# Kernel optimization log

Measured on AMD Instinct MI355X. Metric: run time of the kernel, lower is better.

## Reference

```python
import jax, jax.numpy as jnp
import numpy as np
import math

B, H, N, T, D, R = 1, 32, 2048, 2048, 128, 64


def setup_inputs() -> dict:
    key = jax.random.key(0)
    k1, k2, k3, k4 = jax.random.split(key, 4)
    q = jax.random.normal(k1, (B, H, N, D), dtype=jnp.float32)
    k_orig = jax.random.normal(k2, (B, H, T, D), dtype=jnp.float32)
    # emulate a quantized key: orig + small perturbation (any float tensor works)
    k_quant = k_orig + 0.05 * jax.random.normal(k3, (B, H, T, D), dtype=jnp.float32)
    # JL projection buffer: randn(dim, rank) / sqrt(rank)
    G = jax.random.normal(k4, (D, R), dtype=jnp.float32) / math.sqrt(R)
    return {"q": q, "k_orig": k_orig, "k_quant": k_quant, "G": G}


def reference(q, k_orig, k_quant, G):
    rank = G.shape[1]
    alpha = 1.0 / math.sqrt(rank)
    # compute_sign: sign of JL-projected residual -> (B,H,T,R), values in {-1,0,+1}
    e = k_orig - k_quant
    s = jnp.sign(jnp.einsum('bhtd,dr->bhtr', e, G))
    # correct_score
    raw_scores = jnp.einsum('bhnd,bhtd->bhnt', q, k_quant)          # (B,H,N,T)
    q_proj = jnp.einsum('bhnd,dr->bhnr', q, G) / math.sqrt(rank)     # (B,H,N,R)
    corr = jnp.einsum('bhnr,bhtr->bhnt', q_proj, s) * alpha          # (B,H,N,T)
    return raw_scores + corr
```

## Files before the change

kernel.cpp:

```cpp
#include <hip/hip_runtime.h>


#define H 32
#define NQ 2048
#define NT 2048
#define D 128
#define R 64
#define KDIM 192

typedef __attribute__((ext_vector_type(4))) float f32x4;
typedef __attribute__((ext_vector_type(8))) short bf16x8;

__device__ __forceinline__ short f2bf(float x) {
  union { float f; unsigned u; } v; v.f = x;
  unsigned r = v.u + 0x7fff + ((v.u >> 16) & 1);
  return (short)(r >> 16);
}
__device__ __forceinline__ float bf2f(short h) {
  union { unsigned u; float f; } v; v.u = ((unsigned)(unsigned short)h) << 16;
  return v.f;
}

__device__ __forceinline__ void gl_lds16(const void* g, void* l) {
  __builtin_amdgcn_global_load_lds(
      (const __attribute__((address_space(1))) void*)g,
      (__attribute__((address_space(3))) void*)l, 16, 0, 0);
}

__global__ __launch_bounds__(256, 2) void prep(
    const float* __restrict__ q, const float* __restrict__ ko,
    const float* __restrict__ kq, const float* __restrict__ G,
    short* __restrict__ Qb, short* __restrict__ Kb) {
  const int tid = threadIdx.x, lane = tid & 63, wave = tid >> 6;
  const int quad = lane >> 4, mrow = lane & 15;
  const bool kmode = blockIdx.x < (H * NT / 128);
  const long blk = kmode ? blockIdx.x : (blockIdx.x - H * NT / 128);
  const long rbase = blk * 128 + wave * 32;
  short* outb = kmode ? Kb : Qb;

  f32x4 acc[2][4] = {};

  for (int ks = 0; ks < 4; ++ks) {
    const int d0 = ks * 32 + quad * 8;
    bf16x8 gh[4], gl[4];
#pragma unroll
    for (int j = 0; j < 4; ++j) {
      const float* gp = G + (size_t)d0 * R + j * 16 + mrow;
#pragma unroll
      for (int e = 0; e < 8; ++e) {
        float g = gp[(size_t)e * R];
        short hb = f2bf(g);
        gh[j][e] = hb;
        gl[j][e] = f2bf(g - bf2f(hb));
      }
    }
    bf16x8 ah[2], al[2];
#pragma unroll
    for (int i = 0; i < 2; ++i) {
      const long row = rbase + i * 16 + mrow;
      if (kmode) {
        const f32x4 a0 = *(const f32x4*)(ko + row * D + d0);
        const f32x4 a1 = *(const f32x4*)(ko + row * D + d0 + 4);
        const f32x4 b0 = *(const f32x4*)(kq + row * D + d0);
        const f32x4 b1 = *(const f32x4*)(kq + row * D + d0 + 4);
        bf16x8 kqb;
#pragma unroll
        for (int t = 0; t < 4; ++t) {
          kqb[t] = f2bf(b0[t]); kqb[t + 4] = f2bf(b1[t]);
          float e0 = a0[t] - b0[t];
          short h0 = f2bf(e0); ah[i][t] = h0; al[i][t] = f2bf(e0 - bf2f(h0));
          float e1 = a1[t] - b1[t];
          short h1 = f2bf(e1); ah[i][t + 4] = h1; al[i][t + 4] = f2bf(e1 - bf2f(h1));
        }
        *(bf16x8*)(Kb + row * KDIM + d0) = kqb;
      } else {
        const f32x4 a0 = *(const f32x4*)(q + row * D + d0);
        const f32x4 a1 = *(const f32x4*)(q + row * D + d0 + 4);
        bf16x8 qb;
#pragma unroll
        for (int t = 0; t < 4; ++t) {
          short h0 = f2bf(a0[t]); qb[t] = h0; ah[i][t] = h0; al[i][t] = 0;
          short h1 = f2bf(a1[t]); qb[t + 4] = h1; ah[i][t + 4] = h1; al[i][t + 4] = 0;
        }
        *(bf16x8*)(Qb + row * KDIM + d0) = qb;
      }
    }
#pragma unroll
    for (int i = 0; i < 2; ++i)
#pragma unroll
      for (int j = 0; j < 4; ++j) {
        acc[i][j] = __builtin_amdgcn_mfma_f32_16x16x32_bf16(ah[i], gh[j], acc[i][j], 0, 0, 0);
        if (kmode) {
          acc[i][j] = __builtin_amdgcn_mfma_f32_16x16x32_bf16(al[i], gh[j], acc[i][j], 0, 0, 0);
          acc[i][j] = __builtin_amdgcn_mfma_f32_16x16x32_bf16(ah[i], gl[j], acc[i][j], 0, 0, 0);
        }
      }
  }
#pragma unroll
  for (int i = 0; i < 2; ++i)
#pragma unroll
    for (int j = 0; j < 4; ++j)
#pragma unroll
      for (int r = 0; r < 4; ++r) {
        const long row = rbase + i * 16 + quad * 4 + r;
        const int col = j * 16 + mrow;
        float v = acc[i][j][r];
        short s;
        if (kmode)
          s = v > 0.f ? (short)0x3C80 : (v < 0.f ? (short)0xBC80 : (short)0);
        else
          s = f2bf(v);
        outb[row * KDIM + 128 + col] = s;
      }
}

__global__ __launch_bounds__(256, 3) void gemm_bt(const short* __restrict__ Qb,
                                                  const short* __restrict__ Kb,
                                                  float* __restrict__ out) {
  const int h  = blockIdx.z;
  const int m0 = blockIdx.y * 128;
  const int n0 = blockIdx.x * 128;
  const short* A = Qb + (size_t)h * NQ * KDIM;
  const short* B = Kb + (size_t)h * NT * KDIM;

  __shared__ __align__(16) short As[2][128 * 32];
  __shared__ __align__(16) short Bs[2][128 * 32];

  const int tid = threadIdx.x, lane = tid & 63, wave = tid >> 6;
  const int wm = (wave >> 1) * 64, wn = (wave & 1) * 64;
  const int quad = lane >> 4, mrow = lane & 15;

  f32x4 acc[4][4] = {};

  const int srow = tid >> 2;
  const int scol = (tid & 3) * 8;
  const short* gA  = A + (size_t)(m0 + srow) * KDIM + scol;
  const short* gA2 = A + (size_t)(m0 + 64 + srow) * KDIM + scol;
  const short* gB  = B + (size_t)(n0 + srow) * KDIM + scol;
  const short* gB2 = B + (size_t)(n0 + 64 + srow) * KDIM + scol;

  auto stage = [&](int b, int kt) {
    char* a1 = (char*)(&As[b][0]) + wave * 1024;
    char* a2 = (char*)(&As[b][0]) + 4096 + wave * 1024;
    char* b1 = (char*)(&Bs[b][0]) + wave * 1024;
    char* b2 = (char*)(&Bs[b][0]) + 4096 + wave * 1024;
    gl_lds16(gA + kt * 32, a1);
    gl_lds16(gA2 + kt * 32, a2);
    gl_lds16(gB + kt * 32, b1);
    gl_lds16(gB2 + kt * 32, b2);
  };

  stage(0, 0);
  asm volatile("s_waitcnt vmcnt(0)" ::: "memory");
  __builtin_amdgcn_s_barrier();

#pragma unroll
  for (int kt = 0; kt < 6; ++kt) {
    const int cur = kt & 1;
    if (kt < 5) stage(cur ^ 1, kt + 1);

    bf16x8 af[4], bfv[4];
#pragma unroll
    for (int i = 0; i < 4; ++i) {
      af[i]  = *(const bf16x8*)((const char*)(&As[cur][0]) + (wm + i * 16 + mrow) * 64 + quad * 16);
      bfv[i] = *(const bf16x8*)((const char*)(&Bs[cur][0]) + (wn + i * 16 + mrow) * 64 + quad * 16);
    }
#pragma unroll
    for (int i = 0; i < 4; ++i)
#pragma unroll
      for (int j = 0; j < 4; ++j)
        acc[i][j] = __builtin_amdgcn_mfma_f32_16x16x32_bf16(af[i], bfv[j], acc[i][j], 0, 0, 0);

    if (kt < 5) {
      asm volatile("s_waitcnt vmcnt(0)" ::: "memory");
      __builtin_amdgcn_s_barrier();
    }
  }

  float* orow = out + ((size_t)h * NQ + m0) * NT + n0;
#pragma unroll
  for (int i = 0; i < 4; ++i)
#pragma unroll
    for (int r = 0; r < 4; ++r) {
      const int row = wm + i * 16 + quad * 4 + r;
      float* p = orow + (size_t)row * NT + wn + mrow;
#pragma unroll
      for (int j = 0; j < 4; ++j) p[j * 16] = acc[i][j][r];
    }
}

extern "C" void kernel_launch(void* const* d_in, const int* in_sizes, int n_in,
                              void* d_out, int out_size, void* d_ws, size_t ws_size,
                              hipStream_t stream) {
  const float* q  = (const float*)d_in[0];
  const float* ko = (const float*)d_in[1];
  const float* kq = (const float*)d_in[2];
  const float* G  = (const float*)d_in[3];
  float* out = (float*)d_out;

  short* Kb = (short*)d_ws;
  short* Qb = Kb + (size_t)H * NT * KDIM;

  prep<<<(H * NT + H * NQ) / 128, 256, 0, stream>>>(q, ko, kq, G, Qb, Kb);

  dim3 grid(NT / 128, NQ / 128, H);
  gemm_bt<<<grid, 256, 0, stream>>>(Qb, Kb, out);
}
```

Before: 678.6 us.

## Replace LDS-tiled GEMM with register-resident A strip streaming over all K tiles

The GEMM now launches 512 blocks of 512 threads. Each block owns a 128-row Q strip for one head and holds the full 192-wide A fragments in registers. It loops over all 16 key tiles, loading B fragments directly from global memory with a two-half software prefetch, and writes each 128x128 output tile with nontemporal stores. This removes LDS staging, barriers and repeated A loads, and the block index is swizzled so heads interleave. The cost is heavy register pressure and uncoalesced direct global B loads that depend on cache reuse across waves.

After: 684.9 us. No clear change (+0.9%).

```diff
diff --git a/kernel.cpp b/kernel.cpp
--- a/kernel.cpp
+++ b/kernel.cpp
@@ -19,12 +19,6 @@
 __device__ __forceinline__ float bf2f(short h) {
   union { unsigned u; float f; } v; v.u = ((unsigned)(unsigned short)h) << 16;
   return v.f;
-}
-
-__device__ __forceinline__ void gl_lds16(const void* g, void* l) {
-  __builtin_amdgcn_global_load_lds(
-      (const __attribute__((address_space(1))) void*)g,
-      (__attribute__((address_space(3))) void*)l, 16, 0, 0);
 }
 
 __global__ __launch_bounds__(256, 2) void prep(
@@ -114,79 +108,86 @@
       }
 }
 
-__global__ __launch_bounds__(256, 3) void gemm_bt(const short* __restrict__ Qb,
-                                                  const short* __restrict__ Kb,
-                                                  float* __restrict__ out) {
-  const int h  = blockIdx.z;
-  const int m0 = blockIdx.y * 128;
-  const int n0 = blockIdx.x * 128;
+__global__ __launch_bounds__(512, 2) void gemm_strip(const short* __restrict__ Qb,
+                                                     const short* __restrict__ Kb,
+                                                     float* __restrict__ out) {
+  const int bid = blockIdx.x;
+  const int h = (bid & 7) + ((bid >> 3) & 3) * 8;
+  const int m0 = (bid >> 5) * 128;
+
+  const int tid = threadIdx.x, lane = tid & 63, wave = tid >> 6;
+  const int quad = lane >> 4, mrow = lane & 15;
+  const int wm = (wave >> 2) * 64;
+  const int wn = (wave & 3) * 32;
+
   const short* A = Qb + (size_t)h * NQ * KDIM;
   const short* B = Kb + (size_t)h * NT * KDIM;
 
-  __shared__ __align__(16) short As[2][128 * 32];
-  __shared__ __align__(16) short Bs[2][128 * 32];
-
-  const int tid = threadIdx.x, lane = tid & 63, wave = tid >> 6;
-  const int wm = (wave >> 1) * 64, wn = (wave & 1) * 64;
-  const int quad = lane >> 4, mrow = lane & 15;
-
-  f32x4 acc[4][4] = {};
-
-  const int srow = tid >> 2;
-  const int scol = (tid & 3) * 8;
-  const short* gA  = A + (size_t)(m0 + srow) * KDIM + scol;
-  const short* gA2 = A + (size_t)(m0 + 64 + srow) * KDIM + scol;
-  const short* gB  = B + (size_t)(n0 + srow) * KDIM + scol;
-  const short* gB2 = B + (size_t)(n0 + 64 + srow) * KDIM + scol;
-
-  auto stage = [&](int b, int kt) {
-    char* a1 = (char*)(&As[b][0]) + wave * 1024;
-    char* a2 = (char*)(&As[b][0]) + 4096 + wave * 1024;
-    char* b1 = (char*)(&Bs[b][0]) + wave * 1024;
-    char* b2 = (char*)(&Bs[b][0]) + 4096 + wave * 1024;
-    gl_lds16(gA + kt * 32, a1);
-    gl_lds16(gA2 + kt * 32, a2);
-    gl_lds16(gB + kt * 32, b1);
-    gl_lds16(gB2 + kt * 32, b2);
-  };
-
-  stage(0, 0);
-  asm volatile("s_waitcnt vmcnt(0)" ::: "memory");
-  __builtin_amdgcn_s_barrier();
-
-#pragma unroll
-  for (int kt = 0; kt < 6; ++kt) {
-    const int cur = kt & 1;
-    if (kt < 5) stage(cur ^ 1, kt + 1);
-
-    bf16x8 af[4], bfv[4];
-#pragma unroll
-    for (int i = 0; i < 4; ++i) {
-      af[i]  = *(const bf16x8*)((const char*)(&As[cur][0]) + (wm + i * 16 + mrow) * 64 + quad * 16);
-      bfv[i] = *(const bf16x8*)((const char*)(&Bs[cur][0]) + (wn + i * 16 + mrow) * 64 + quad * 16);
+  bf16x8 af[4][6];
+#pragma unroll
+  for (int i = 0; i < 4; ++i) {
+    const short* ap = A + (size_t)(m0 + wm + i * 16 + mrow) * KDIM + quad * 8;
+#pragma unroll
+    for (int kc = 0; kc < 6; ++kc) af[i][kc] = *(const bf16x8*)(ap + kc * 32);
+  }
+
+  const short* bbase = B + (size_t)(wn + mrow) * KDIM + quad * 8;
+
+  f32x4 acc[4][2] = {};
+  bf16x8 b0[2][3], b1[2][3];
+
+#pragma unroll
+  for (int j = 0; j < 2; ++j)
+#pragma unroll
+    for (int kc = 0; kc < 3; ++kc)
+      b0[j][kc] = *(const bf16x8*)(bbase + (size_t)j * 16 * KDIM + kc * 32);
+
+  float* obase = out + ((size_t)h * NQ + m0 + wm + quad * 4) * NT + wn + mrow;
+
+#pragma unroll 1
+  for (int t = 0; t < NT / 128; ++t) {
+    const short* bt = bbase + (size_t)t * 128 * KDIM;
+#pragma unroll
+    for (int j = 0; j < 2; ++j)
+#pragma unroll
+      for (int kc = 0; kc < 3; ++kc)
+        b1[j][kc] = *(const bf16x8*)(bt + (size_t)j * 16 * KDIM + (kc + 3) * 32);
+#pragma unroll
+    for (int kc = 0; kc < 3; ++kc)
+#pragma unroll
+      for (int i = 0; i < 4; ++i)
+#pragma unroll
+        for (int j = 0; j < 2; ++j)
+          acc[i][j] = __builtin_amdgcn_mfma_f32_16x16x32_bf16(af[i][kc], b0[j][kc], acc[i][j], 0, 0, 0);
+    if (t < NT / 128 - 1) {
+      const short* bn = bt + (size_t)128 * KDIM;
+#pragma unroll
+      for (int j = 0; j < 2; ++j)
+#pragma unroll
+        for (int kc = 0; kc < 3; ++kc)
+          b0[j][kc] = *(const bf16x8*)(bn + (size_t)j * 16 * KDIM + kc * 32);
     }
 #pragma unroll
+    for (int kc = 0; kc < 3; ++kc)
+#pragma unroll
+      for (int i = 0; i < 4; ++i)
+#pragma unroll
+        for (int j = 0; j < 2; ++j)
+          acc[i][j] = __builtin_amdgcn_mfma_f32_16x16x32_bf16(af[i][kc + 3], b1[j][kc], acc[i][j], 0, 0, 0);
+    float* op = obase + t * 128;
+#pragma unroll
     for (int i = 0; i < 4; ++i)
 #pragma unroll
-      for (int j = 0; j < 4; ++j)
-        acc[i][j] = __builtin_amdgcn_mfma_f32_16x16x32_bf16(af[i], bfv[j], acc[i][j], 0, 0, 0);
-
-    if (kt < 5) {
-      asm volatile("s_waitcnt vmcnt(0)" ::: "memory");
-      __builtin_amdgcn_s_barrier();
-    }
+      for (int r = 0; r < 4; ++r) {
+        float* p = op + (size_t)(i * 16 + r) * NT;
+#pragma unroll
+        for (int j = 0; j < 2; ++j) __builtin_nontemporal_store(acc[i][j][r], p + j * 16);
+      }
+#pragma unroll
+    for (int i = 0; i < 4; ++i)
+#pragma unroll
+      for (int j = 0; j < 2; ++j) acc[i][j] = (f32x4){0.f, 0.f, 0.f, 0.f};
   }
-
-  float* orow = out + ((size_t)h * NQ + m0) * NT + n0;
-#pragma unroll
-  for (int i = 0; i < 4; ++i)
-#pragma unroll
-    for (int r = 0; r < 4; ++r) {
-      const int row = wm + i * 16 + quad * 4 + r;
-      float* p = orow + (size_t)row * NT + wn + mrow;
-#pragma unroll
-      for (int j = 0; j < 4; ++j) p[j * 16] = acc[i][j][r];
-    }
 }
 
 extern "C" void kernel_launch(void* const* d_in, const int* in_sizes, int n_in,
@@ -203,6 +204,5 @@
 
   prep<<<(H * NT + H * NQ) / 128, 256, 0, stream>>>(q, ko, kq, G, Qb, Kb);
 
-  dim3 grid(NT / 128, NQ / 128, H);
-  gemm_bt<<<grid, 256, 0, stream>>>(Qb, Kb, out);
-}
+  gemm_strip<<<512, 512, 0, stream>>>(Qb, Kb, out);
+}
```
